# Kernel optimization log

Hardware: AMD Instinct MI355X
Metric: run time of the kernel (lower is better)

Reference implementation:

```python
import jax, jax.numpy as jnp
import numpy as np

P = 1024   # number of partitions / local models (n_terms)
K = 9      # local neighborhood size (in_dim of each LocalDNN)
W = 10     # LocalDNN width
B = 16384  # batch
F = 1024   # input feature dim (lattice sites)


def setup_inputs() -> dict:
    key = jax.random.key(0)
    ks = jax.random.split(key, 9)
    x = jax.random.normal(ks[0], (B, F), dtype=jnp.float32)
    idx = jax.random.randint(ks[1], (P, K), 0, F)  # parameter_map: per-partition feature indices
    # stacked LocalDNN parameters (one tiny MLP per partition)
    s1 = 1.0 / np.sqrt(K)
    s2 = 1.0 / np.sqrt(W)
    W1 = jax.random.uniform(ks[2], (P, K, W), jnp.float32, -s1, s1)
    b1 = jax.random.uniform(ks[3], (P, W), jnp.float32, -s1, s1)
    W2 = jax.random.uniform(ks[4], (P, W, W), jnp.float32, -s2, s2)
    b2 = jax.random.uniform(ks[5], (P, W), jnp.float32, -s2, s2)
    W3 = jax.random.uniform(ks[6], (P, W), jnp.float32, -s2, s2)   # Linear(width,1) weight
    b3 = jax.random.uniform(ks[7], (P,), jnp.float32, -s2, s2)
    sP = 1.0 / np.sqrt(P)
    w_last = jax.random.uniform(ks[8], (P,), jnp.float32, -sP, sP)  # Linear(n_terms,1,bias=False)
    return {"x": x, "idx": idx, "W1": W1, "b1": b1, "W2": W2, "b2": b2,
            "W3": W3, "b3": b3, "w_last": w_last}


def reference(x, idx, W1, b1, W2, b2, W3, b3, w_last):
    # local_map: gather per-partition features -> [B, P, K]
    xg = x[:, idx]
    # LocalDNN (depth=2): Linear(K,W) -> tanh -> Linear(W,W) -> (dropout eval no-op) -> Linear(W,1)
    h = jnp.tanh(jnp.einsum('bpk,pkw->bpw', xg, W1) + b1)      # [B,P,W]
    h = jnp.einsum('bpw,pwv->bpv', h, W2) + b2                  # [B,P,W]
    local_out = jnp.einsum('bpw,pw->bp', h, W3) + b3            # concat of per-model outputs [B,P]
    y = local_out @ w_last                                      # last_layer, flatten -> [B]
    return jnp.stack((y, jnp.full_like(y, jnp.sum(jnp.abs(w_last)))))
```

## Files before the change

kernel.cpp:

```cpp
#include <hip/hip_runtime.h>
#include <cstdint>
#include <cstddef>

#define B_TOT   16384
#define F_DIM   1024
#define P_TOT   1024
#define K_IN    9
#define W_H     10
#define TB      128
#define THREADS 1024
#define NWAVE   16
#define PGRP    2
#define PPB     (P_TOT / PGRP)
#define LSTR    1028

#define REC_DW   64
#define TANH_C   2.8853900817779268f
#define F8_MAX   448.0f

typedef float f32x2 __attribute__((ext_vector_type(2)));

__device__ __forceinline__ float fast_exp2(float x) {
#if __has_builtin(__builtin_amdgcn_exp2f)
    return __builtin_amdgcn_exp2f(x);
#else
    return exp2f(x);
#endif
}
__device__ __forceinline__ float fast_rcp(float x) {
#if __has_builtin(__builtin_amdgcn_rcpf)
    return __builtin_amdgcn_rcpf(x);
#else
    return 1.0f / x;
#endif
}
__device__ __forceinline__ float sigm_r(float z) {
    return fast_rcp(fast_exp2(z) + 1.0f);
}
__device__ __forceinline__ f32x2 pkfma(f32x2 a, f32x2 b, f32x2 c) {
#if __has_builtin(__builtin_elementwise_fma)
    return __builtin_elementwise_fma(a, b, c);
#else
    return f32x2{fmaf(a[0], b[0], c[0]), fmaf(a[1], b[1], c[1])};
#endif
}
__device__ __forceinline__ f32x2 unpk8_w0(uint32_t u) {
#if __has_builtin(__builtin_amdgcn_cvt_pk_f32_fp8)
    auto v = __builtin_amdgcn_cvt_pk_f32_fp8((int)u, false);
    return f32x2{v[0], v[1]};
#else
    return f32x2{__builtin_amdgcn_cvt_f32_fp8((int)u, 0),
                 __builtin_amdgcn_cvt_f32_fp8((int)u, 1)};
#endif
}
__device__ __forceinline__ f32x2 unpk8_w1(uint32_t u) {
#if __has_builtin(__builtin_amdgcn_cvt_pk_f32_fp8)
    auto v = __builtin_amdgcn_cvt_pk_f32_fp8((int)u, true);
    return f32x2{v[0], v[1]};
#else
    return f32x2{__builtin_amdgcn_cvt_f32_fp8((int)u, 2),
                 __builtin_amdgcn_cvt_f32_fp8((int)u, 3)};
#endif
}
__device__ __forceinline__ f32x2 unpk8s(uint32_t u, int word) {
    return word ? unpk8_w1(u) : unpk8_w0(u);
}
__device__ __forceinline__ uint32_t pk2(float a0, float a1, float b0, float b1) {
    uint32_t u = (uint32_t)__builtin_amdgcn_cvt_pk_fp8_f32(a0, a1, 0, false);
    u = (uint32_t)__builtin_amdgcn_cvt_pk_fp8_f32(b0, b1, (int)u, true);
    return u;
}
__device__ __forceinline__ uint32_t comp4(const uint4& c, int j) {
    switch (j & 3) { case 0: return c.x; case 1: return c.y;
                     case 2: return c.z; default: return c.w; }
}
__device__ __forceinline__ uint32_t cvdw(const uint4* cv, int d) {
    return comp4(cv[d >> 2], d & 3);
}
__device__ __forceinline__ float cvf(const uint4* cv, int d) {
    return __uint_as_float(cvdw(cv, d));
}
__device__ __forceinline__ void ld_cv(uint4* dst, const uint32_t* recp) {
    const uint4* rv = reinterpret_cast<const uint4*>(recp);
    asm("" : "+v"(rv));
    #pragma unroll
    for (int i = 0; i < 11; ++i) dst[i] = rv[i];
}

__device__ __forceinline__ uint32_t rec_dword(
    int p, int dw, const int* idx,
    const float* w1, const float* b1, const float* w2, const float* b2,
    const float* w3, const float* b3, const float* wl,
    float s1, float q1)
{
    if (dw < 9)  return (uint32_t)idx[p * 9 + dw];
    if (dw == 9) return __float_as_uint(s1 * TANH_C);
    if (dw < 20) return __float_as_uint(b1[p * 10 + (dw - 10)] * TANH_C);
    if (dw < 43) {
        const int d = dw - 20, t0 = 2 * d, t1 = t0 + 1;
        const int e0 = (t0 / 5) * 10 + 2 * (t0 % 5);
        const float a0 = w1[e0] * q1, a1 = w1[e0 + 1] * q1;
        float bq0 = 0.f, bq1 = 0.f;
        if (t1 < 45) {
            const int e1 = (t1 / 5) * 10 + 2 * (t1 % 5);
            bq0 = w1[e1] * q1; bq1 = w1[e1 + 1] * q1;
        }
        return pk2(a0, a1, bq0, bq1);
    }
    if (dw < 48) return 0;
    if (dw == 48) {
        float bb = b3[p];
        for (int v = 0; v < 10; ++v) bb = fmaf(b2[p * 10 + v], w3[v], bb);
        float s = 0.f;
        for (int w = 0; w < 10; ++w)
            for (int v = 0; v < 10; ++v)
                s = fmaf(w2[w * 10 + v], w3[v], s);
        return __float_as_uint(wl[p] * (s + bb));
    }
    if (dw == 49) return 0;
    if (dw < 60) {
        const int w = dw - 50;
        float s = 0.f;
        for (int v = 0; v < 10; ++v) s = fmaf(w2[w * 10 + v], w3[v], s);
        return __float_as_uint(-2.0f * wl[p] * s);
    }
    return 0;
}

__global__ __launch_bounds__(64)
void prep_quant(const int* __restrict__ idx,
                const float* __restrict__ W1, const float* __restrict__ b1,
                const float* __restrict__ W2, const float* __restrict__ b2,
                const float* __restrict__ W3, const float* __restrict__ b3,
                const float* __restrict__ wl, uint32_t* __restrict__ ws)
{
    const int p = blockIdx.x;
    const int l = threadIdx.x;
    const float* w1 = W1 + p * 90;
    const float* w2 = W2 + p * 100;
    const float* w3 = W3 + p * 10;

    float m1 = (l < 90) ? fabsf(w1[l]) : 0.0f;
    if (l + 64 < 90) m1 = fmaxf(m1, fabsf(w1[l + 64]));
    #pragma unroll
    for (int off = 32; off > 0; off >>= 1)
        m1 = fmaxf(m1, __shfl_xor(m1, off));
    m1 = fmaxf(m1, 1e-20f);
    const float s1 = m1 / F8_MAX, q1 = F8_MAX / m1;

    ws[(size_t)p * REC_DW + l] =
        rec_dword(p, l, idx, w1, b1, w2, b2, w3, b3, wl, s1, q1);
}

__global__ __launch_bounds__(THREADS, 4)
void dnn_q8(const float* __restrict__ x, const uint32_t* __restrict__ ws,
            const float* __restrict__ wl, float* __restrict__ out)
{
    extern __shared__ unsigned char xs[];
    __shared__ float partial[NWAVE][TB];

    const int tid = threadIdx.x;
    const int b0  = blockIdx.x * TB;
    const int p0  = blockIdx.y * PPB;

    #pragma unroll
    for (int i = 0; i < (TB * (F_DIM / 4)) / THREADS; ++i) {
        const int q   = i * THREADS + tid;
        const int row = q >> 8;
        const int c4  = q & 255;
        const float4 v = *reinterpret_cast<const float4*>(
            x + (size_t)(b0 + row) * F_DIM + (c4 << 2));
        int pk = __builtin_amdgcn_cvt_pk_fp8_f32(v.x, v.y, 0, false);
        pk     = __builtin_amdgcn_cvt_pk_fp8_f32(v.z, v.w, pk, true);
        *reinterpret_cast<uint32_t*>(xs + row * LSTR + (c4 << 2)) = (uint32_t)pk;
    }
    __syncthreads();

    const int lane = tid & 63;
    const int wave = tid >> 6;
    const unsigned char* __restrict__ row0 = xs + lane * LSTR;
    const unsigned char* __restrict__ row1 = xs + (lane + 64) * LSTR;

    float y0 = 0.0f, y1 = 0.0f;

    for (int jp = 0; jp < PPB / NWAVE; ++jp) {
        const int p  = p0 + jp * NWAVE + wave;
        const int pu = __builtin_amdgcn_readfirstlane(p);
        const float* __restrict__ rfs =
            reinterpret_cast<const float*>(ws + (size_t)pu * REC_DW);
        uint4 cv[11];
        ld_cv(cv, ws + (size_t)p * REC_DW);

        float xg0[K_IN], xg1[K_IN];
        #pragma unroll
        for (int k = 0; k < K_IN; ++k) {
            const int c = (int)cvdw(cv, k);
            xg0[k] = __builtin_amdgcn_cvt_f32_fp8((int)row0[c], 0);
            xg1[k] = __builtin_amdgcn_cvt_f32_fp8((int)row1[c], 0);
        }

        f32x2 H0[5], H1[5];
        #pragma unroll
        for (int j = 0; j < 5; ++j) { H0[j] = f32x2{0.f, 0.f}; H1[j] = f32x2{0.f, 0.f}; }
        #pragma unroll
        for (int k = 0; k < K_IN; ++k) {
            const f32x2 xa = {xg0[k], xg0[k]};
            const f32x2 xb = {xg1[k], xg1[k]};
            #pragma unroll
            for (int j = 0; j < 5; ++j) {
                const int t = k * 5 + j;
                const f32x2 w = unpk8s(cvdw(cv, 20 + (t >> 1)), t & 1);
                H0[j] = pkfma(xa, w, H0[j]);
                H1[j] = pkfma(xb, w, H1[j]);
            }
        }
        const float s1c = cvf(cv, 9);
        const f32x2 s1p = {s1c, s1c};
        f32x2 r0[5], r1[5];
        #pragma unroll
        for (int j = 0; j < 5; ++j) {
            const f32x2 bj = {cvf(cv, 10 + 2 * j), cvf(cv, 11 + 2 * j)};
            const f32x2 z0 = pkfma(H0[j], s1p, bj);
            const f32x2 z1 = pkfma(H1[j], s1p, bj);
            r0[j] = f32x2{sigm_r(z0[0]), sigm_r(z0[1])};
            r1[j] = f32x2{sigm_r(z1[0]), sigm_r(z1[1])};
        }

        const float c0 = rfs[48];
        f32x2 A0 = {0.f, 0.f}, A1 = {0.f, 0.f};
        #pragma unroll
        for (int j = 0; j < 5; ++j) {
            const f32x2 cwj = {rfs[50 + 2 * j], rfs[51 + 2 * j]};
            A0 = pkfma(cwj, r0[j], A0);
            A1 = pkfma(cwj, r1[j], A1);
        }
        y0 += c0 + A0[0] + A0[1];
        y1 += c0 + A1[0] + A1[1];
    }

    partial[wave][lane]      = y0;
    partial[wave][lane + 64] = y1;
    __syncthreads();

    if (tid < TB) {
        float s = 0.0f;
        #pragma unroll
        for (int w = 0; w < NWAVE; ++w) s += partial[w][tid];
        atomicAdd(&out[b0 + tid], s);
    }

    if (blockIdx.y == 0 && tid < 64) {
        float sa = 0.0f;
        #pragma unroll
        for (int i = 0; i < P_TOT / 64; ++i) sa += fabsf(wl[tid + 64 * i]);
        #pragma unroll
        for (int off = 32; off > 0; off >>= 1) sa += __shfl_down(sa, off);
        sa = __shfl(sa, 0);
        out[B_TOT + b0 + tid]      = sa;
        out[B_TOT + b0 + 64 + tid] = sa;
    }
}

extern "C" void kernel_launch(void* const* d_in, const int* in_sizes, int n_in,
                              void* d_out, int out_size, void* d_ws, size_t ws_size,
                              hipStream_t stream)
{
    const float* x  = (const float*)d_in[0];
    const int*   idx= (const int*)  d_in[1];
    const float* W1 = (const float*)d_in[2];
    const float* b1 = (const float*)d_in[3];
    const float* W2 = (const float*)d_in[4];
    const float* b2 = (const float*)d_in[5];
    const float* W3 = (const float*)d_in[6];
    const float* b3 = (const float*)d_in[7];
    const float* wl = (const float*)d_in[8];
    float* out = (float*)d_out;
    uint32_t* ws = (uint32_t*)d_ws;

    (void)hipMemsetAsync(out, 0, B_TOT * sizeof(float), stream);

    prep_quant<<<P_TOT, 64, 0, stream>>>(idx, W1, b1, W2, b2, W3, b3, wl, ws);

    const int smem = TB * LSTR;
    (void)hipFuncSetAttribute(reinterpret_cast<const void*>(dnn_q8),
                              hipFuncAttributeMaxDynamicSharedMemorySize, smem);

    dim3 grid(B_TOT / TB, PGRP);
    dnn_q8<<<grid, THREADS, smem, stream>>>(x, ws, wl, out);
}
```

Before: 109.6 us.

## Reorder weight records for scalar loads and double-buffer packed FP8 weights

Reorders each partition's record so that indices, biases and the folded output coefficients sit in the first 32 dwords. These are now read through a wave-uniform pointer, which allows scalar loads. Only the 24 dwords of packed FP8 W1 weights are loaded per lane as vectors. The partition loop is unrolled by two so the next partition's packed weights are prefetched while the current one is computed, hiding global-load latency. The price is two live register buffers for the weights. The final prefetch also reads one record past this block's partition range, which for the last partition group runs past the end of the workspace.

```diff
diff --git a/kernel.cpp b/kernel.cpp
--- a/kernel.cpp
+++ b/kernel.cpp
@@ -77,14 +77,11 @@
 __device__ __forceinline__ uint32_t cvdw(const uint4* cv, int d) {
     return comp4(cv[d >> 2], d & 3);
 }
-__device__ __forceinline__ float cvf(const uint4* cv, int d) {
-    return __uint_as_float(cvdw(cv, d));
-}
-__device__ __forceinline__ void ld_cv(uint4* dst, const uint32_t* recp) {
-    const uint4* rv = reinterpret_cast<const uint4*>(recp);
+__device__ __forceinline__ void ld_cv6(uint4* dst, const uint32_t* recp32) {
+    const uint4* rv = reinterpret_cast<const uint4*>(recp32);
     asm("" : "+v"(rv));
     #pragma unroll
-    for (int i = 0; i < 11; ++i) dst[i] = rv[i];
+    for (int i = 0; i < 6; ++i) dst[i] = rv[i];
 }
 
 __device__ __forceinline__ uint32_t rec_dword(
@@ -96,8 +93,24 @@
     if (dw < 9)  return (uint32_t)idx[p * 9 + dw];
     if (dw == 9) return __float_as_uint(s1 * TANH_C);
     if (dw < 20) return __float_as_uint(b1[p * 10 + (dw - 10)] * TANH_C);
-    if (dw < 43) {
-        const int d = dw - 20, t0 = 2 * d, t1 = t0 + 1;
+    if (dw == 20) {
+        float bb = b3[p];
+        for (int v = 0; v < 10; ++v) bb = fmaf(b2[p * 10 + v], w3[v], bb);
+        float s = 0.f;
+        for (int w = 0; w < 10; ++w)
+            for (int v = 0; v < 10; ++v)
+                s = fmaf(w2[w * 10 + v], w3[v], s);
+        return __float_as_uint(wl[p] * (s + bb));
+    }
+    if (dw < 31) {
+        const int w = dw - 21;
+        float s = 0.f;
+        for (int v = 0; v < 10; ++v) s = fmaf(w2[w * 10 + v], w3[v], s);
+        return __float_as_uint(-2.0f * wl[p] * s);
+    }
+    if (dw < 32) return 0;
+    if (dw < 55) {
+        const int d = dw - 32, t0 = 2 * d, t1 = t0 + 1;
         const int e0 = (t0 / 5) * 10 + 2 * (t0 % 5);
         const float a0 = w1[e0] * q1, a1 = w1[e0 + 1] * q1;
         float bq0 = 0.f, bq1 = 0.f;
@@ -107,23 +120,6 @@
         }
         return pk2(a0, a1, bq0, bq1);
     }
-    if (dw < 48) return 0;
-    if (dw == 48) {
-        float bb = b3[p];
-        for (int v = 0; v < 10; ++v) bb = fmaf(b2[p * 10 + v], w3[v], bb);
-        float s = 0.f;
-        for (int w = 0; w < 10; ++w)
-            for (int v = 0; v < 10; ++v)
-                s = fmaf(w2[w * 10 + v], w3[v], s);
-        return __float_as_uint(wl[p] * (s + bb));
-    }
-    if (dw == 49) return 0;
-    if (dw < 60) {
-        const int w = dw - 50;
-        float s = 0.f;
-        for (int v = 0; v < 10; ++v) s = fmaf(w2[w * 10 + v], w3[v], s);
-        return __float_as_uint(-2.0f * wl[p] * s);
-    }
     return 0;
 }
 
@@ -150,6 +146,59 @@
 
     ws[(size_t)p * REC_DW + l] =
         rec_dword(p, l, idx, w1, b1, w2, b2, w3, b3, wl, s1, q1);
+}
+
+__device__ __forceinline__ void visit(
+    const uint32_t* __restrict__ recs, const float* __restrict__ rfs,
+    const uint4* cv,
+    const unsigned char* __restrict__ row0, const unsigned char* __restrict__ row1,
+    float& y0, float& y1)
+{
+    float xg0[K_IN], xg1[K_IN];
+    #pragma unroll
+    for (int k = 0; k < K_IN; ++k) {
+        const int c = (int)recs[k];
+        xg0[k] = __builtin_amdgcn_cvt_f32_fp8((int)row0[c], 0);
+        xg1[k] = __builtin_amdgcn_cvt_f32_fp8((int)row1[c], 0);
+    }
+
+    f32x2 H0[5], H1[5];
+    #pragma unroll
+    for (int j = 0; j < 5; ++j) { H0[j] = f32x2{0.f, 0.f}; H1[j] = f32x2{0.f, 0.f}; }
+    #pragma unroll
+    for (int k = 0; k < K_IN; ++k) {
+        const f32x2 xa = {xg0[k], xg0[k]};
+        const f32x2 xb = {xg1[k], xg1[k]};
+        #pragma unroll
+        for (int j = 0; j < 5; ++j) {
+            const int t = k * 5 + j;
+            const f32x2 w = unpk8s(cvdw(cv, t >> 1), t & 1);
+            H0[j] = pkfma(xa, w, H0[j]);
+            H1[j] = pkfma(xb, w, H1[j]);
+        }
+    }
+    const float s1c = rfs[9];
+    const f32x2 s1p = {s1c, s1c};
+    f32x2 r0[5], r1[5];
+    #pragma unroll
+    for (int j = 0; j < 5; ++j) {
+        const f32x2 bj = {rfs[10 + 2 * j], rfs[11 + 2 * j]};
+        const f32x2 z0 = pkfma(H0[j], s1p, bj);
+        const f32x2 z1 = pkfma(H1[j], s1p, bj);
+        r0[j] = f32x2{sigm_r(z0[0]), sigm_r(z0[1])};
+        r1[j] = f32x2{sigm_r(z1[0]), sigm_r(z1[1])};
+    }
+
+    const float c0 = rfs[20];
+    f32x2 A0 = {0.f, 0.f}, A1 = {0.f, 0.f};
+    #pragma unroll
+    for (int j = 0; j < 5; ++j) {
+        const f32x2 cwj = {rfs[21 + 2 * j], rfs[22 + 2 * j]};
+        A0 = pkfma(cwj, r0[j], A0);
+        A1 = pkfma(cwj, r1[j], A1);
+    }
+    y0 += c0 + A0[0] + A0[1];
+    y1 += c0 + A1[0] + A1[1];
 }
 
 __global__ __launch_bounds__(THREADS, 4)
@@ -183,59 +232,22 @@
 
     float y0 = 0.0f, y1 = 0.0f;
 
-    for (int jp = 0; jp < PPB / NWAVE; ++jp) {
-        const int p  = p0 + jp * NWAVE + wave;
-        const int pu = __builtin_amdgcn_readfirstlane(p);
-        const float* __restrict__ rfs =
-            reinterpret_cast<const float*>(ws + (size_t)pu * REC_DW);
-        uint4 cv[11];
-        ld_cv(cv, ws + (size_t)p * REC_DW);
-
-        float xg0[K_IN], xg1[K_IN];
-        #pragma unroll
-        for (int k = 0; k < K_IN; ++k) {
-            const int c = (int)cvdw(cv, k);
-            xg0[k] = __builtin_amdgcn_cvt_f32_fp8((int)row0[c], 0);
-            xg1[k] = __builtin_amdgcn_cvt_f32_fp8((int)row1[c], 0);
-        }
-
-        f32x2 H0[5], H1[5];
-        #pragma unroll
-        for (int j = 0; j < 5; ++j) { H0[j] = f32x2{0.f, 0.f}; H1[j] = f32x2{0.f, 0.f}; }
-        #pragma unroll
-        for (int k = 0; k < K_IN; ++k) {
-            const f32x2 xa = {xg0[k], xg0[k]};
-            const f32x2 xb = {xg1[k], xg1[k]};
-            #pragma unroll
-            for (int j = 0; j < 5; ++j) {
-                const int t = k * 5 + j;
-                const f32x2 w = unpk8s(cvdw(cv, 20 + (t >> 1)), t & 1);
-                H0[j] = pkfma(xa, w, H0[j]);
-                H1[j] = pkfma(xb, w, H1[j]);
-            }
-        }
-        const float s1c = cvf(cv, 9);
-        const f32x2 s1p = {s1c, s1c};
-        f32x2 r0[5], r1[5];
-        #pragma unroll
-        for (int j = 0; j < 5; ++j) {
-            const f32x2 bj = {cvf(cv, 10 + 2 * j), cvf(cv, 11 + 2 * j)};
-            const f32x2 z0 = pkfma(H0[j], s1p, bj);
-            const f32x2 z1 = pkfma(H1[j], s1p, bj);
-            r0[j] = f32x2{sigm_r(z0[0]), sigm_r(z0[1])};
-            r1[j] = f32x2{sigm_r(z1[0]), sigm_r(z1[1])};
-        }
-
-        const float c0 = rfs[48];
-        f32x2 A0 = {0.f, 0.f}, A1 = {0.f, 0.f};
-        #pragma unroll
-        for (int j = 0; j < 5; ++j) {
-            const f32x2 cwj = {rfs[50 + 2 * j], rfs[51 + 2 * j]};
-            A0 = pkfma(cwj, r0[j], A0);
-            A1 = pkfma(cwj, r1[j], A1);
-        }
-        y0 += c0 + A0[0] + A0[1];
-        y1 += c0 + A1[0] + A1[1];
+    uint4 cvA[6], cvB[6];
+    ld_cv6(cvA, ws + (size_t)(p0 + wave) * REC_DW + 32);
+
+    for (int jp = 0; jp < PPB / NWAVE; jp += 2) {
+        const int pA = p0 + jp * NWAVE + wave;
+        const int pB = pA + NWAVE;
+        const int puA = __builtin_amdgcn_readfirstlane(pA);
+        const int puB = __builtin_amdgcn_readfirstlane(pB);
+        const uint32_t* __restrict__ recsA = ws + (size_t)puA * REC_DW;
+        const uint32_t* __restrict__ recsB = ws + (size_t)puB * REC_DW;
+
+        ld_cv6(cvB, ws + (size_t)pB * REC_DW + 32);
+        visit(recsA, reinterpret_cast<const float*>(recsA), cvA, row0, row1, y0, y1);
+
+        ld_cv6(cvA, ws + (size_t)(pB + NWAVE) * REC_DW + 32);
+        visit(recsB, reinterpret_cast<const float*>(recsB), cvB, row0, row1, y0, y1);
     }
 
     partial[wave][lane]      = y0;
```

Result: no change. 110.1 us (+0.5%).
